# Performance work log

Measured on AMD Instinct MI355X. Metric: run time of the kernel, lower is better.

Reference implementation:

```python
import jax, jax.numpy as jnp
import numpy as np

H, A, V = 8, 32, 32
NODE_IN, EDGE_IN, NODE_OUT, EDGE_OUT = 128, 64, 128, 64


def setup_inputs() -> dict:
    key = jax.random.key(0)
    ks = jax.random.split(key, 8)
    B, N = 1, 384
    s = lambda fan: 1.0 / np.sqrt(fan).astype(np.float32)
    nodes = jax.random.normal(ks[0], (B, NODE_IN, N), jnp.float32)
    edges = jax.random.normal(ks[1], (B, EDGE_IN, N, N), jnp.float32)
    mask = jax.random.randint(ks[2], (B, N), 0, 2).astype(bool)
    W_q = jax.random.normal(ks[3], (A * H, NODE_IN), jnp.float32) * s(NODE_IN)
    W_k = jax.random.normal(ks[4], (A * H, NODE_IN + EDGE_IN), jnp.float32) * s(NODE_IN + EDGE_IN)
    W_v = jax.random.normal(ks[5], (V * H, NODE_IN + EDGE_IN), jnp.float32) * s(NODE_IN + EDGE_IN)
    W_o = jax.random.normal(ks[6], (NODE_OUT, V * H), jnp.float32) * s(V * H)
    W_e = jax.random.normal(ks[7], (EDGE_OUT, V * H + EDGE_IN), jnp.float32) * s(V * H + EDGE_IN)
    return dict(nodes=nodes, edges=edges, mask=mask, W_q=W_q, W_k=W_k, W_v=W_v, W_o=W_o, W_e=W_e)


def reference(nodes, edges, mask, W_q, W_k, W_v, W_o, W_e):
    B, C, N = nodes.shape
    # 1x1 convs are channel matmuls
    query = jnp.einsum('oc,bcn->bon', W_q, nodes)                      # [B, H*A, N]
    node_edges = jnp.concatenate(
        [jnp.broadcast_to(nodes[:, :, :, None], (B, C, N, N)), edges], axis=1)  # [B, C+E, N, N]
    key = jnp.einsum('oc,bcij->boij', W_k, node_edges)                 # [B, H*A, N, N]
    value = jnp.einsum('oc,bcij->boij', W_v, node_edges).reshape(B, H, V, N, N)
    # elementwise QK: query broadcast over column axis j
    sim = (query[:, :, :, None] * key).reshape(B, H, A, N, N).sum(axis=2)
    sim = sim / jnp.sqrt(jnp.asarray(A, sim.dtype))                    # [B, H, N, N]
    sim = jnp.where(mask[:, None, None, :], sim, -jnp.inf)
    sim = jax.nn.softmax(sim, axis=-1)
    mm = (mask[:, None, :, None] & mask[:, None, None, :]).astype(sim.dtype)  # [B,1,N,N]
    sim = sim * mm
    value = value * mm[:, None]
    node_features = jnp.einsum('bhij,bhvij->bhvi', sim, value).reshape(B, H * V, N)
    node_out = jnp.einsum('od,bdn->bon', W_o, node_features)           # [B, node_out, N]
    # symmetrized edge features: (f_i + f_j) / 2, then concat raw edges
    ef = (node_features[:, :, :, None] + node_features[:, :, None, :]) * 0.5  # [B,H*V,N,N]
    ef = jnp.concatenate([ef, edges], axis=1)
    edge_out = jnp.einsum('oc,bcij->boij', W_e, ef)                    # [B, edge_out, N, N]
    return node_out, edge_out
```

## Files before the change

kernel.cpp:

```cpp
#include <hip/hip_runtime.h>
#include <math.h>

#define NN 384
#define NSQ (NN*NN)

#define WS_MASKF 0
#define WS_C1    384
#define WS_P     3456
#define WS_VN    200064
#define WS_T     298368
#define WS_GH    494976
#define WS_WT    519552
#define WS_WOT   523648
#define WS_WVE   556416
#define WS_WEN   572800

typedef short short8 __attribute__((ext_vector_type(8)));
typedef float f32x4 __attribute__((ext_vector_type(4)));

__device__ __forceinline__ unsigned short f2bf(float x) {
    unsigned u = __float_as_uint(x);
    return (unsigned short)((u + 0x7FFFu + ((u >> 16) & 1u)) >> 16);
}

__global__ __launch_bounds__(256) void k_proj(
    const float* __restrict__ nodes, const float* __restrict__ Wq,
    const float* __restrict__ Wk, const float* __restrict__ Wv,
    const float* __restrict__ Wo, const float* __restrict__ We,
    const unsigned int* __restrict__ mi, float* __restrict__ ws) {
    int tid = threadIdx.x;
    if (blockIdx.x >= 48) {
        if (blockIdx.x == 48) {
            __shared__ int bytemode;
            if (tid == 0) bytemode = 0;
            __syncthreads();
            unsigned v0 = mi[tid];
            unsigned v1 = (tid < 128) ? mi[256 + tid] : 0u;
            if (v0 > 1u || v1 > 1u) bytemode = 1;
            __syncthreads();
            float* maskf = ws + WS_MASKF;
            for (int j = tid; j < NN; j += 256) {
                int on;
                if (bytemode) on = (((const unsigned char*)mi)[j] != 0);
                else          on = (mi[j] != 0u);
                maskf[j] = on ? 1.0f : 0.0f;
            }
        } else if (blockIdx.x == 49) {
            unsigned short* WtBF = reinterpret_cast<unsigned short*>(ws + WS_WT);
            for (int idx = tid; idx < 4096; idx += 256) {
                int o = idx >> 6, c = idx & 63;
                WtBF[o * 64 + c] = f2bf(We[o * 320 + 256 + c]);
            }
        } else if (blockIdx.x == 50) {
            float* WoT = ws + WS_WOT;
            for (int idx = tid; idx < 32768; idx += 256) {
                int dd = idx >> 7, o = idx & 127;
                WoT[dd * 128 + o] = Wo[o * 256 + dd];
            }
        } else if (blockIdx.x == 51) {
            float* WvE = ws + WS_WVE;
            for (int idx = tid; idx < 16384; idx += 256) {
                int c = idx >> 8, d = idx & 255;
                WvE[c * 256 + d] = Wv[d * 192 + 128 + c];
            }
        } else {
            float* WeN = ws + WS_WEN;
            for (int idx = tid; idx < 16384; idx += 256) {
                int dd = idx >> 6, o = idx & 63;
                WeN[dd * 64 + o] = We[o * 320 + dd];
            }
        }
        return;
    }
    float* c1_ws = ws + WS_C1;
    float* P_ws  = ws + WS_P;
    float* vn_ws = ws + WS_VN;
    int i0 = blockIdx.x * 8;
    __shared__ float nl[128][8];
    __shared__ float q_l[256][8];
    __shared__ float qk_l[256][8];
    for (int idx = tid; idx < 1024; idx += 256) {
        int m = idx >> 3, ii = idx & 7;
        nl[m][ii] = nodes[m * NN + i0 + ii];
    }
    __syncthreads();
    int o = tid;
    float aq[8], ak[8], av[8];
#pragma unroll
    for (int ii = 0; ii < 8; ii++) { aq[ii] = 0.f; ak[ii] = 0.f; av[ii] = 0.f; }
#pragma unroll 4
    for (int m = 0; m < 128; m++) {
        float wq = Wq[o * 128 + m];
        float wk = Wk[o * 192 + m];
        float wv = Wv[o * 192 + m];
#pragma unroll
        for (int ii = 0; ii < 8; ii++) {
            float nv = nl[m][ii];
            aq[ii] = fmaf(wq, nv, aq[ii]);
            ak[ii] = fmaf(wk, nv, ak[ii]);
            av[ii] = fmaf(wv, nv, av[ii]);
        }
    }
#pragma unroll
    for (int ii = 0; ii < 8; ii++) {
        vn_ws[(size_t)(i0 + ii) * 256 + o] = av[ii];
        q_l[o][ii]  = aq[ii];
        qk_l[o][ii] = aq[ii] * ak[ii];
    }
    __syncthreads();
    if (tid < 64) {
        int h = tid >> 3, ii = tid & 7;
        float s = 0.f;
        for (int a = 0; a < 32; a++) s += qk_l[h * 32 + a][ii];
        c1_ws[(i0 + ii) * 8 + h] = s;
    }
    for (int rep = 0; rep < 2; rep++) {
        int idx = rep * 256 + tid;
        int c = idx & 63, h = idx >> 6;
        float ap[8];
#pragma unroll
        for (int ii = 0; ii < 8; ii++) ap[ii] = 0.f;
        for (int a = 0; a < 32; a++) {
            float w = Wk[(h * 32 + a) * 192 + 128 + c];
#pragma unroll
            for (int ii = 0; ii < 8; ii++)
                ap[ii] = fmaf(q_l[h * 32 + a][ii], w, ap[ii]);
        }
#pragma unroll
        for (int ii = 0; ii < 8; ii++)
            P_ws[(size_t)(i0 + ii) * 512 + c * 8 + h] = ap[ii];
    }
}

__global__ __launch_bounds__(512) void k_attn(
    const float* __restrict__ edges, const float* __restrict__ ws_ro,
    float* __restrict__ T_ws) {
    __shared__ __align__(16) unsigned short epad_h[64 * 392];
    __shared__ __align__(16) float sT2[NN * 8];
    const float* maskf = ws_ro + WS_MASKF;
    const float* c1w   = ws_ro + WS_C1;
    const float* Pw    = ws_ro + WS_P;
    int i = blockIdx.x;
    int tid = threadIdx.x;
    int wv = tid >> 6, ln = tid & 63;
    float mask_i = maskf[i];

    if (tid < NN) {
        int j = tid;
        const float* eb = edges + (size_t)i * NN + j;
        const float* Pi = Pw + (size_t)i * 512;
        float acc[8];
#pragma unroll
        for (int h = 0; h < 8; h++) acc[h] = 0.f;
#pragma unroll
        for (int cb = 0; cb < 4; cb++) {
            float ev[16];
#pragma unroll
            for (int t = 0; t < 16; t++)
                ev[t] = eb[(size_t)(cb * 16 + t) * NSQ];
#pragma unroll
            for (int t = 0; t < 16; t++) {
                int c = cb * 16 + t;
                epad_h[c * 392 + j] = f2bf(ev[t]);
                const float* Pc = Pi + c * 8;
#pragma unroll
                for (int h = 0; h < 8; h++) acc[h] = fmaf(Pc[h], ev[t], acc[h]);
            }
        }
        float mj = maskf[j];
        const float* c1i = c1w + i * 8;
        float sv[8];
#pragma unroll
        for (int h = 0; h < 8; h++) {
            float s = (c1i[h] + acc[h]) * 0.17677669529663687f;
            sv[h] = (mj != 0.0f) ? s : -1e30f;
        }
        *reinterpret_cast<float4*>(&sT2[j * 8])     = make_float4(sv[0], sv[1], sv[2], sv[3]);
        *reinterpret_cast<float4*>(&sT2[j * 8 + 4]) = make_float4(sv[4], sv[5], sv[6], sv[7]);
    }
    __syncthreads();
    float v[6];
    {
        int h = wv;
#pragma unroll
        for (int k = 0; k < 6; k++) v[k] = sT2[(ln + 64 * k) * 8 + h];
    }
    __syncthreads();
    {
        int h = wv;
        float m = v[0];
#pragma unroll
        for (int k = 1; k < 6; k++) m = fmaxf(m, v[k]);
#pragma unroll
        for (int s = 1; s < 64; s <<= 1) m = fmaxf(m, __shfl_xor(m, s));
        float ex[6]; float sum = 0.f;
#pragma unroll
        for (int k = 0; k < 6; k++) { ex[k] = __expf(v[k] - m); sum += ex[k]; }
#pragma unroll
        for (int s = 1; s < 64; s <<= 1) sum += __shfl_xor(sum, s);
        float fac = mask_i / sum;
        unsigned short* s_bf = reinterpret_cast<unsigned short*>(sT2);
#pragma unroll
        for (int k = 0; k < 6; k++)
            s_bf[h * 392 + ln + 64 * k] = f2bf(ex[k] * fac);
    }
    __syncthreads();
    if (tid < 64) {
        const unsigned short* s_bf = reinterpret_cast<const unsigned short*>(sT2);
        int L = tid;
        int nc   = L & 15;
        int quad = L >> 4;
        int hrow = nc & 7;
        f32x4 acc0 = {0.f, 0.f, 0.f, 0.f};
        f32x4 acc1 = {0.f, 0.f, 0.f, 0.f};
        f32x4 acc2 = {0.f, 0.f, 0.f, 0.f};
        f32x4 acc3 = {0.f, 0.f, 0.f, 0.f};
#pragma unroll
        for (int s = 0; s < 12; s++) {
            int jb = s * 32 + quad * 8;
            short8 a = *reinterpret_cast<const short8*>(&s_bf[hrow * 392 + jb]);
            short8 b0 = *reinterpret_cast<const short8*>(&epad_h[(0 * 16 + nc) * 392 + jb]);
            short8 b1 = *reinterpret_cast<const short8*>(&epad_h[(1 * 16 + nc) * 392 + jb]);
            short8 b2 = *reinterpret_cast<const short8*>(&epad_h[(2 * 16 + nc) * 392 + jb]);
            short8 b3 = *reinterpret_cast<const short8*>(&epad_h[(3 * 16 + nc) * 392 + jb]);
            acc0 = __builtin_amdgcn_mfma_f32_16x16x32_bf16(a, b0, acc0, 0, 0, 0);
            acc1 = __builtin_amdgcn_mfma_f32_16x16x32_bf16(a, b1, acc1, 0, 0, 0);
            acc2 = __builtin_amdgcn_mfma_f32_16x16x32_bf16(a, b2, acc2, 0, 0, 0);
            acc3 = __builtin_amdgcn_mfma_f32_16x16x32_bf16(a, b3, acc3, 0, 0, 0);
        }
        if (L < 32) {
            float* To = T_ws + (size_t)i * 512;
#pragma unroll
            for (int r = 0; r < 4; r++) {
                int h = quad * 4 + r;
                To[h * 64 +  0 + nc] = acc0[r];
                To[h * 64 + 16 + nc] = acc1[r];
                To[h * 64 + 32 + nc] = acc2[r];
                To[h * 64 + 48 + nc] = acc3[r];
            }
        }
    }
}

__global__ __launch_bounds__(256) void k_nf(
    const float* __restrict__ ws_ro, float* __restrict__ gh_ws,
    float* __restrict__ out) {
    const float* maskf = ws_ro + WS_MASKF;
    const float* vn_ws = ws_ro + WS_VN;
    const float* T_ws  = ws_ro + WS_T;
    const float* WvE   = ws_ro + WS_WVE;
    const float* WoT   = ws_ro + WS_WOT;
    const float* WeN   = ws_ro + WS_WEN;
    int i = blockIdx.x, tid = threadIdx.x;
    __shared__ float T_l[512];
    __shared__ float nf_l[256];
    T_l[tid]       = T_ws[(size_t)i * 512 + tid];
    T_l[tid + 256] = T_ws[(size_t)i * 512 + 256 + tid];
    __syncthreads();
    int d = tid, h = d >> 5;
    float a0 = 0.f, a1 = 0.f, a2 = 0.f, a3 = 0.f;
#pragma unroll
    for (int c = 0; c < 64; c += 4) {
        a0 = fmaf(WvE[(c    ) * 256 + d], T_l[h * 64 + c    ], a0);
        a1 = fmaf(WvE[(c + 1) * 256 + d], T_l[h * 64 + c + 1], a1);
        a2 = fmaf(WvE[(c + 2) * 256 + d], T_l[h * 64 + c + 2], a2);
        a3 = fmaf(WvE[(c + 3) * 256 + d], T_l[h * 64 + c + 3], a3);
    }
    nf_l[d] = maskf[i] * vn_ws[(size_t)i * 256 + d] + ((a0 + a1) + (a2 + a3));
    __syncthreads();
    if (tid < 128) {
        int o = tid;
        float b0 = 0.f, b1 = 0.f, b2 = 0.f, b3 = 0.f;
#pragma unroll 8
        for (int dd = 0; dd < 256; dd += 4) {
            b0 = fmaf(WoT[(dd    ) * 128 + o], nf_l[dd    ], b0);
            b1 = fmaf(WoT[(dd + 1) * 128 + o], nf_l[dd + 1], b1);
            b2 = fmaf(WoT[(dd + 2) * 128 + o], nf_l[dd + 2], b2);
            b3 = fmaf(WoT[(dd + 3) * 128 + o], nf_l[dd + 3], b3);
        }
        out[o * NN + i] = (b0 + b1) + (b2 + b3);
    } else if (tid < 192) {
        int o = tid - 128;
        float b0 = 0.f, b1 = 0.f, b2 = 0.f, b3 = 0.f;
#pragma unroll 8
        for (int dd = 0; dd < 256; dd += 4) {
            b0 = fmaf(WeN[(dd    ) * 64 + o], nf_l[dd    ], b0);
            b1 = fmaf(WeN[(dd + 1) * 64 + o], nf_l[dd + 1], b1);
            b2 = fmaf(WeN[(dd + 2) * 64 + o], nf_l[dd + 2], b2);
            b3 = fmaf(WeN[(dd + 3) * 64 + o], nf_l[dd + 3], b3);
        }
        gh_ws[o * NN + i] = 0.5f * ((b0 + b1) + (b2 + b3));
    }
}

__global__ __launch_bounds__(192) void k_edge(
    const float* __restrict__ edges, const float* __restrict__ ws_ro,
    float* __restrict__ out_e) {
    __shared__ __align__(16) unsigned short eT[192 * 72];
    const unsigned short* WtBF = reinterpret_cast<const unsigned short*>(ws_ro + WS_WT);
    const float* gh = ws_ro + WS_GH;
    int i = blockIdx.x, jh = blockIdx.y, tid = threadIdx.x;

    {
        const float* eb = edges + (size_t)i * NN + jh * 192 + tid;
#pragma unroll
        for (int cb = 0; cb < 4; cb++) {
            float ev[16];
#pragma unroll
            for (int t = 0; t < 16; t++)
                ev[t] = eb[(size_t)(cb * 16 + t) * NSQ];
            short8 p0, p1;
#pragma unroll
            for (int t = 0; t < 8; t++) p0[t] = (short)f2bf(ev[t]);
#pragma unroll
            for (int t = 0; t < 8; t++) p1[t] = (short)f2bf(ev[t + 8]);
            *reinterpret_cast<short8*>(&eT[tid * 72 + cb * 16])     = p0;
            *reinterpret_cast<short8*>(&eT[tid * 72 + cb * 16 + 8]) = p1;
        }
    }
    __syncthreads();

    int L = tid & 63, wv = tid >> 6;
    int nc = L & 15, quad = L >> 4;
    short8 a00 = *reinterpret_cast<const short8*>(&WtBF[(0 * 16 + nc) * 64 + 0  + quad * 8]);
    short8 a01 = *reinterpret_cast<const short8*>(&WtBF[(0 * 16 + nc) * 64 + 32 + quad * 8]);
    short8 a10 = *reinterpret_cast<const short8*>(&WtBF[(1 * 16 + nc) * 64 + 0  + quad * 8]);
    short8 a11 = *reinterpret_cast<const short8*>(&WtBF[(1 * 16 + nc) * 64 + 32 + quad * 8]);
    short8 a20 = *reinterpret_cast<const short8*>(&WtBF[(2 * 16 + nc) * 64 + 0  + quad * 8]);
    short8 a21 = *reinterpret_cast<const short8*>(&WtBF[(2 * 16 + nc) * 64 + 32 + quad * 8]);
    short8 a30 = *reinterpret_cast<const short8*>(&WtBF[(3 * 16 + nc) * 64 + 0  + quad * 8]);
    short8 a31 = *reinterpret_cast<const short8*>(&WtBF[(3 * 16 + nc) * 64 + 32 + quad * 8]);
    float ghi[16];
#pragma unroll
    for (int ot = 0; ot < 4; ot++)
#pragma unroll
        for (int r = 0; r < 4; r++)
            ghi[ot * 4 + r] = gh[(ot * 16 + quad * 4 + r) * NN + i];

#pragma unroll
    for (int jj = 0; jj < 4; jj++) {
        int jt = wv * 4 + jj;
        short8 b0 = *reinterpret_cast<const short8*>(&eT[(jt * 16 + nc) * 72 + 0  + quad * 8]);
        short8 b1 = *reinterpret_cast<const short8*>(&eT[(jt * 16 + nc) * 72 + 32 + quad * 8]);
        int j = jh * 192 + jt * 16 + nc;
        f32x4 c0 = {0.f, 0.f, 0.f, 0.f};
        f32x4 c1 = {0.f, 0.f, 0.f, 0.f};
        f32x4 c2 = {0.f, 0.f, 0.f, 0.f};
        f32x4 c3 = {0.f, 0.f, 0.f, 0.f};
        c0 = __builtin_amdgcn_mfma_f32_16x16x32_bf16(a00, b0, c0, 0, 0, 0);
        c0 = __builtin_amdgcn_mfma_f32_16x16x32_bf16(a01, b1, c0, 0, 0, 0);
        c1 = __builtin_amdgcn_mfma_f32_16x16x32_bf16(a10, b0, c1, 0, 0, 0);
        c1 = __builtin_amdgcn_mfma_f32_16x16x32_bf16(a11, b1, c1, 0, 0, 0);
        c2 = __builtin_amdgcn_mfma_f32_16x16x32_bf16(a20, b0, c2, 0, 0, 0);
        c2 = __builtin_amdgcn_mfma_f32_16x16x32_bf16(a21, b1, c2, 0, 0, 0);
        c3 = __builtin_amdgcn_mfma_f32_16x16x32_bf16(a30, b0, c3, 0, 0, 0);
        c3 = __builtin_amdgcn_mfma_f32_16x16x32_bf16(a31, b1, c3, 0, 0, 0);
#pragma unroll
        for (int ot = 0; ot < 4; ot++) {
            f32x4 cc = ot == 0 ? c0 : ot == 1 ? c1 : ot == 2 ? c2 : c3;
#pragma unroll
            for (int r = 0; r < 4; r++) {
                int o = ot * 16 + quad * 4 + r;
                float val = cc[r] + ghi[ot * 4 + r] + gh[o * NN + j];
                __builtin_nontemporal_store(val, &out_e[(size_t)o * NSQ + (size_t)i * NN + j]);
            }
        }
    }
}

extern "C" void kernel_launch(void* const* d_in, const int* in_sizes, int n_in,
                              void* d_out, int out_size, void* d_ws, size_t ws_size,
                              hipStream_t stream) {
    const float* nodes = (const float*)d_in[0];
    const float* edges = (const float*)d_in[1];
    const unsigned int* mask = (const unsigned int*)d_in[2];
    const float* Wq = (const float*)d_in[3];
    const float* Wk = (const float*)d_in[4];
    const float* Wv = (const float*)d_in[5];
    const float* Wo = (const float*)d_in[6];
    const float* We = (const float*)d_in[7];
    float* out = (float*)d_out;
    float* ws  = (float*)d_ws;
    float* out_e = out + 128 * NN;

    hipLaunchKernelGGL(k_proj, dim3(53), dim3(256), 0, stream,
                       nodes, Wq, Wk, Wv, Wo, We, mask, ws);
    hipLaunchKernelGGL(k_attn, dim3(384), dim3(512), 0, stream,
                       edges, ws, ws + WS_T);
    hipLaunchKernelGGL(k_nf, dim3(384), dim3(256), 0, stream, ws,
                       ws + WS_GH, out);
    hipLaunchKernelGGL(k_edge, dim3(384, 2), dim3(192), 0, stream,
                       edges, ws, out_e);
}
```

Before: 159.4 us.

## Fuse node-feature projection into attention kernel and spread MFMA across four waves

Merges the k_nf kernel into k_attn. The per-row T result now stays in LDS instead of taking a global round trip, and one kernel launch is removed. The MFMA aggregation stage, which used a single wave, is split so four waves each compute one 16-column output slice. The cost is more LDS per block and extra barriers in k_attn, which may lower occupancy slightly.

Result: faster. 155.9 us (-2.2%).

```diff
diff --git a/kernel.cpp b/kernel.cpp
--- a/kernel.cpp
+++ b/kernel.cpp
@@ -134,12 +134,18 @@
 
 __global__ __launch_bounds__(512) void k_attn(
     const float* __restrict__ edges, const float* __restrict__ ws_ro,
-    float* __restrict__ T_ws) {
+    float* __restrict__ gh_ws, float* __restrict__ out) {
     __shared__ __align__(16) unsigned short epad_h[64 * 392];
     __shared__ __align__(16) float sT2[NN * 8];
+    __shared__ __align__(16) float T_lds[512];
+    __shared__ float nf_lds[256];
     const float* maskf = ws_ro + WS_MASKF;
     const float* c1w   = ws_ro + WS_C1;
     const float* Pw    = ws_ro + WS_P;
+    const float* vn_ws = ws_ro + WS_VN;
+    const float* WvE   = ws_ro + WS_WVE;
+    const float* WoT   = ws_ro + WS_WOT;
+    const float* WeN   = ws_ro + WS_WEN;
     int i = blockIdx.x;
     int tid = threadIdx.x;
     int wv = tid >> 6, ln = tid & 63;
@@ -205,78 +211,50 @@
             s_bf[h * 392 + ln + 64 * k] = f2bf(ex[k] * fac);
     }
     __syncthreads();
-    if (tid < 64) {
+    if (tid < 256) {
         const unsigned short* s_bf = reinterpret_cast<const unsigned short*>(sT2);
-        int L = tid;
-        int nc   = L & 15;
-        int quad = L >> 4;
+        int nc   = ln & 15;
+        int quad = ln >> 4;
         int hrow = nc & 7;
-        f32x4 acc0 = {0.f, 0.f, 0.f, 0.f};
-        f32x4 acc1 = {0.f, 0.f, 0.f, 0.f};
-        f32x4 acc2 = {0.f, 0.f, 0.f, 0.f};
-        f32x4 acc3 = {0.f, 0.f, 0.f, 0.f};
+        f32x4 acc = {0.f, 0.f, 0.f, 0.f};
 #pragma unroll
         for (int s = 0; s < 12; s++) {
             int jb = s * 32 + quad * 8;
             short8 a = *reinterpret_cast<const short8*>(&s_bf[hrow * 392 + jb]);
-            short8 b0 = *reinterpret_cast<const short8*>(&epad_h[(0 * 16 + nc) * 392 + jb]);
-            short8 b1 = *reinterpret_cast<const short8*>(&epad_h[(1 * 16 + nc) * 392 + jb]);
-            short8 b2 = *reinterpret_cast<const short8*>(&epad_h[(2 * 16 + nc) * 392 + jb]);
-            short8 b3 = *reinterpret_cast<const short8*>(&epad_h[(3 * 16 + nc) * 392 + jb]);
-            acc0 = __builtin_amdgcn_mfma_f32_16x16x32_bf16(a, b0, acc0, 0, 0, 0);
-            acc1 = __builtin_amdgcn_mfma_f32_16x16x32_bf16(a, b1, acc1, 0, 0, 0);
-            acc2 = __builtin_amdgcn_mfma_f32_16x16x32_bf16(a, b2, acc2, 0, 0, 0);
-            acc3 = __builtin_amdgcn_mfma_f32_16x16x32_bf16(a, b3, acc3, 0, 0, 0);
-        }
-        if (L < 32) {
-            float* To = T_ws + (size_t)i * 512;
+            short8 b = *reinterpret_cast<const short8*>(&epad_h[(wv * 16 + nc) * 392 + jb]);
+            acc = __builtin_amdgcn_mfma_f32_16x16x32_bf16(a, b, acc, 0, 0, 0);
+        }
+        if (ln < 32) {
 #pragma unroll
             for (int r = 0; r < 4; r++) {
                 int h = quad * 4 + r;
-                To[h * 64 +  0 + nc] = acc0[r];
-                To[h * 64 + 16 + nc] = acc1[r];
-                To[h * 64 + 32 + nc] = acc2[r];
-                To[h * 64 + 48 + nc] = acc3[r];
-            }
-        }
-    }
-}
-
-__global__ __launch_bounds__(256) void k_nf(
-    const float* __restrict__ ws_ro, float* __restrict__ gh_ws,
-    float* __restrict__ out) {
-    const float* maskf = ws_ro + WS_MASKF;
-    const float* vn_ws = ws_ro + WS_VN;
-    const float* T_ws  = ws_ro + WS_T;
-    const float* WvE   = ws_ro + WS_WVE;
-    const float* WoT   = ws_ro + WS_WOT;
-    const float* WeN   = ws_ro + WS_WEN;
-    int i = blockIdx.x, tid = threadIdx.x;
-    __shared__ float T_l[512];
-    __shared__ float nf_l[256];
-    T_l[tid]       = T_ws[(size_t)i * 512 + tid];
-    T_l[tid + 256] = T_ws[(size_t)i * 512 + 256 + tid];
-    __syncthreads();
-    int d = tid, h = d >> 5;
-    float a0 = 0.f, a1 = 0.f, a2 = 0.f, a3 = 0.f;
-#pragma unroll
-    for (int c = 0; c < 64; c += 4) {
-        a0 = fmaf(WvE[(c    ) * 256 + d], T_l[h * 64 + c    ], a0);
-        a1 = fmaf(WvE[(c + 1) * 256 + d], T_l[h * 64 + c + 1], a1);
-        a2 = fmaf(WvE[(c + 2) * 256 + d], T_l[h * 64 + c + 2], a2);
-        a3 = fmaf(WvE[(c + 3) * 256 + d], T_l[h * 64 + c + 3], a3);
-    }
-    nf_l[d] = maskf[i] * vn_ws[(size_t)i * 256 + d] + ((a0 + a1) + (a2 + a3));
+                T_lds[h * 64 + wv * 16 + nc] = acc[r];
+            }
+        }
+    }
+    __syncthreads();
+    if (tid < 256) {
+        int d = tid, h = d >> 5;
+        float a0 = 0.f, a1 = 0.f, a2 = 0.f, a3 = 0.f;
+#pragma unroll
+        for (int c = 0; c < 64; c += 4) {
+            a0 = fmaf(WvE[(c    ) * 256 + d], T_lds[h * 64 + c    ], a0);
+            a1 = fmaf(WvE[(c + 1) * 256 + d], T_lds[h * 64 + c + 1], a1);
+            a2 = fmaf(WvE[(c + 2) * 256 + d], T_lds[h * 64 + c + 2], a2);
+            a3 = fmaf(WvE[(c + 3) * 256 + d], T_lds[h * 64 + c + 3], a3);
+        }
+        nf_lds[d] = mask_i * vn_ws[(size_t)i * 256 + d] + ((a0 + a1) + (a2 + a3));
+    }
     __syncthreads();
     if (tid < 128) {
         int o = tid;
         float b0 = 0.f, b1 = 0.f, b2 = 0.f, b3 = 0.f;
 #pragma unroll 8
         for (int dd = 0; dd < 256; dd += 4) {
-            b0 = fmaf(WoT[(dd    ) * 128 + o], nf_l[dd    ], b0);
-            b1 = fmaf(WoT[(dd + 1) * 128 + o], nf_l[dd + 1], b1);
-            b2 = fmaf(WoT[(dd + 2) * 128 + o], nf_l[dd + 2], b2);
-            b3 = fmaf(WoT[(dd + 3) * 128 + o], nf_l[dd + 3], b3);
+            b0 = fmaf(WoT[(dd    ) * 128 + o], nf_lds[dd    ], b0);
+            b1 = fmaf(WoT[(dd + 1) * 128 + o], nf_lds[dd + 1], b1);
+            b2 = fmaf(WoT[(dd + 2) * 128 + o], nf_lds[dd + 2], b2);
+            b3 = fmaf(WoT[(dd + 3) * 128 + o], nf_lds[dd + 3], b3);
         }
         out[o * NN + i] = (b0 + b1) + (b2 + b3);
     } else if (tid < 192) {
@@ -284,10 +262,10 @@
         float b0 = 0.f, b1 = 0.f, b2 = 0.f, b3 = 0.f;
 #pragma unroll 8
         for (int dd = 0; dd < 256; dd += 4) {
-            b0 = fmaf(WeN[(dd    ) * 64 + o], nf_l[dd    ], b0);
-            b1 = fmaf(WeN[(dd + 1) * 64 + o], nf_l[dd + 1], b1);
-            b2 = fmaf(WeN[(dd + 2) * 64 + o], nf_l[dd + 2], b2);
-            b3 = fmaf(WeN[(dd + 3) * 64 + o], nf_l[dd + 3], b3);
+            b0 = fmaf(WeN[(dd    ) * 64 + o], nf_lds[dd    ], b0);
+            b1 = fmaf(WeN[(dd + 1) * 64 + o], nf_lds[dd + 1], b1);
+            b2 = fmaf(WeN[(dd + 2) * 64 + o], nf_lds[dd + 2], b2);
+            b3 = fmaf(WeN[(dd + 3) * 64 + o], nf_lds[dd + 3], b3);
         }
         gh_ws[o * NN + i] = 0.5f * ((b0 + b1) + (b2 + b3));
     }
@@ -386,9 +364,7 @@
     hipLaunchKernelGGL(k_proj, dim3(53), dim3(256), 0, stream,
                        nodes, Wq, Wk, Wv, Wo, We, mask, ws);
     hipLaunchKernelGGL(k_attn, dim3(384), dim3(512), 0, stream,
-                       edges, ws, ws + WS_T);
-    hipLaunchKernelGGL(k_nf, dim3(384), dim3(256), 0, stream, ws,
-                       ws + WS_GH, out);
+                       edges, ws, ws + WS_GH, out);
     hipLaunchKernelGGL(k_edge, dim3(384, 2), dim3(192), 0, stream,
                        edges, ws, out_e);
 }
```
